# Kernel optimization log

Hardware: AMD Instinct MI355X
Metric: run time of the kernel (lower is better)

Reference implementation:

```python
import jax, jax.numpy as jnp
import numpy as np

N_NODES = 20000
N_EDGES = 640000
N_GRAPHS = 64
HID = 256
NF = 128
NG = 100   # edge_channels / num_gaussians
NBLK = 6
CUTOFF = 10.0
LOG2 = float(np.log(2.0))


def setup_inputs() -> dict:
    key = jax.random.key(0)
    ks = jax.random.split(key, 24)
    inp = {}
    inp['atom_types'] = jax.random.randint(ks[0], (N_NODES,), 0, 100)
    inp['edge_index'] = jax.random.randint(ks[1], (2, N_EDGES), 0, N_NODES)
    inp['edge_length'] = jax.random.uniform(ks[2], (N_EDGES, 1), jnp.float32) * CUTOFF
    inp['batch_seg'] = jnp.sort(jax.random.randint(ks[3], (N_NODES,), 0, N_GRAPHS))
    s = 0.05
    # embedding table (Embedding(100, hidden); init small so max_norm=10 renorm is inactive)
    inp['atom_emb'] = jax.random.normal(ks[4], (100, HID), jnp.float32) * 0.5
    # per-interaction-block params, stacked on a leading block axis; weights stored [in, out]
    inp['W1s'] = jax.random.normal(ks[5], (NBLK, NG, NF), jnp.float32) * s      # filter MLP lin1
    inp['b1s'] = jnp.zeros((NBLK, NF), jnp.float32)
    inp['W2s'] = jax.random.normal(ks[6], (NBLK, NF, NF), jnp.float32) * s      # filter MLP lin2
    inp['b2s'] = jnp.zeros((NBLK, NF), jnp.float32)
    inp['lin1Ws'] = jax.random.normal(ks[7], (NBLK, HID, NF), jnp.float32) * s  # CFConv.lin1 (no bias)
    inp['lin2Ws'] = jax.random.normal(ks[8], (NBLK, NF, HID), jnp.float32) * s  # CFConv.lin2
    inp['lin2bs'] = jnp.zeros((NBLK, HID), jnp.float32)
    inp['linWs'] = jax.random.normal(ks[9], (NBLK, HID, HID), jnp.float32) * s  # InteractionBlock.lin
    inp['linbs'] = jnp.zeros((NBLK, HID), jnp.float32)
    # final MLP: Linear(256,256) -> act -> Linear(256,256)
    inp['fW1'] = jax.random.normal(ks[10], (HID, HID), jnp.float32) * s
    inp['fb1'] = jnp.zeros((HID,), jnp.float32)
    inp['fW2'] = jax.random.normal(ks[11], (HID, HID), jnp.float32) * s
    inp['fb2'] = jnp.zeros((HID,), jnp.float32)
    return inp


def _ssp(x):
    # ShiftedSoftplus: softplus(x) - log(2)
    return jax.nn.softplus(x) - LOG2


def reference(atom_emb, W1s, b1s, W2s, b2s, lin1Ws, lin2Ws, lin2bs, linWs, linbs,
              fW1, fb1, fW2, fb2, edge_length, atom_types, edge_index, batch_seg):
    n = atom_types.shape[0]
    h = atom_emb[atom_types]                                     # [N, H]
    # Gaussian smearing edge encoder: exp(-0.5/dg^2 * (d - mu_k)^2)
    offsets = jnp.linspace(0.0, CUTOFF, NG)
    coeff = -0.5 / (offsets[1] - offsets[0]) ** 2
    edge_attr = jnp.exp(coeff * (edge_length - offsets[None, :]) ** 2)  # [E, NG]
    # smooth=False cutoff gate
    C = (edge_length <= CUTOFF).astype(h.dtype)                  # [E, 1]
    src, dst = edge_index[0], edge_index[1]
    for i in range(NBLK):
        W = _ssp(edge_attr @ W1s[i] + b1s[i]) @ W2s[i] + b2s[i]  # [E, F]
        W = W * C
        xf = h @ lin1Ws[i]                                       # [N, F]
        msg = xf[src] * W                                        # gather + filter: [E, F]
        agg = jax.ops.segment_sum(msg, dst, num_segments=n)      # scatter-add: [N, F]
        hc = _ssp(agg @ lin2Ws[i] + lin2bs[i])
        hc = hc @ linWs[i] + linbs[i]
        h = h + hc                                               # residual
    pooled = jax.ops.segment_max(h, batch_seg, num_segments=N_GRAPHS)  # global_max_pool
    out = jax.nn.relu(pooled @ fW1 + fb1) @ fW2 + fb2
    return out
```

## Files before the change

kernel.cpp:

```cpp
#include <hip/hip_runtime.h>
#include <math.h>

#define HID 256
#define NF 128
#define NGAUSS 100
#define NBLK 6
#define NGRAPH 64
#define CUTOFF_F 10.0f
#define T_TAB 2048

typedef __attribute__((ext_vector_type(8))) short bf16x8;
typedef __attribute__((ext_vector_type(4))) float f32x4;

__device__ __forceinline__ float ssp(float x) {
    return fmaxf(x, 0.0f) + log1pf(expf(-fabsf(x))) - 0.69314718056f;
}
__device__ __forceinline__ short f2bf(float f) {
    unsigned u = __float_as_uint(f);
    u = u + 0x7fffu + ((u >> 16) & 1u);
    return (short)(u >> 16);
}
__device__ __forceinline__ float bf2f(unsigned s) {
    return __uint_as_float(s << 16);
}
__device__ __forceinline__ unsigned enc_f(float f) {
    unsigned b = __float_as_uint(f);
    return (b & 0x80000000u) ? ~b : (b | 0x80000000u);
}
__device__ __forceinline__ float dec_f(unsigned u) {
    unsigned b = (u & 0x80000000u) ? (u & 0x7FFFFFFFu) : ~u;
    return __uint_as_float(b);
}

__global__ __launch_bounds__(256) void transpose_bf(
        const float* __restrict__ in, short* __restrict__ out,
        int K_src, int K_pad, int C)
{
    int i = blockIdx.y;
    int idx = blockIdx.x * 256 + threadIdx.x;
    if (idx >= K_pad * C) return;
    int k = idx / C, c = idx % C;
    out[((size_t)i * C + c) * K_pad + k] =
        (k < K_src) ? f2bf(in[((size_t)i * K_src + k) * C + c]) : (short)0;
}

__global__ __launch_bounds__(256) void build_table_mfma(
        const short* __restrict__ W1T, const float* __restrict__ b1s,
        const short* __restrict__ W2T, const float* __restrict__ b2s,
        short* __restrict__ Wtab)
{
    __shared__ short Gs[32 * NF];
    __shared__ short Hs[32 * NF];
    char* gb = (char*)Gs;
    char* hb = (char*)Hs;
    const int i = blockIdx.y;
    const int r0 = blockIdx.x * 32;
    const int wv = threadIdx.x >> 6, lane = threadIdx.x & 63;
    const int lrow = lane & 15, lgrp = lane >> 4;

    const float delta = CUTOFF_F / 99.0f;
    const float coeff = -0.5f / (delta * delta);
    for (int idx = threadIdx.x; idx < 32 * NF; idx += 256) {
        int row = idx >> 7, k = idx & 127;
        float d = (float)(r0 + row) * (CUTOFF_F / (float)(T_TAB - 1));
        float x = d - (float)k * delta;
        float v = (k < NGAUSS) ? expf(coeff * x * x) : 0.0f;
        int byte = idx * 2;
        byte ^= (row & 7) << 4;
        *(short*)(gb + byte) = f2bf(v);
    }
    __syncthreads();

    f32x4 zero = {0.0f, 0.0f, 0.0f, 0.0f};
    f32x4 c1[2][2] = {{zero, zero}, {zero, zero}};
    for (int s = 0; s < 4; ++s) {
        bf16x8 a[2], b[2];
        #pragma unroll
        for (int m = 0; m < 2; ++m) {
            int row = m * 16 + lrow;
            int byte = (row * NF + s * 32 + lgrp * 8) * 2;
            byte ^= (row & 7) << 4;
            a[m] = *(const bf16x8*)(gb + byte);
        }
        #pragma unroll
        for (int n = 0; n < 2; ++n) {
            int col = wv * 32 + n * 16 + lrow;
            b[n] = *(const bf16x8*)(W1T + ((size_t)i * NF + col) * NF + s * 32 + lgrp * 8);
        }
        #pragma unroll
        for (int m = 0; m < 2; ++m)
            #pragma unroll
            for (int n = 0; n < 2; ++n)
                c1[m][n] = __builtin_amdgcn_mfma_f32_16x16x32_bf16(a[m], b[n], c1[m][n], 0, 0, 0);
    }
    #pragma unroll
    for (int m = 0; m < 2; ++m)
        #pragma unroll
        for (int n = 0; n < 2; ++n) {
            int col = wv * 32 + n * 16 + lrow;
            float bb = b1s[i * NF + col];
            #pragma unroll
            for (int j = 0; j < 4; ++j) {
                int row = m * 16 + lgrp * 4 + j;
                int byte = (row * NF + col) * 2;
                byte ^= (row & 7) << 4;
                *(short*)(hb + byte) = f2bf(ssp(c1[m][n][j] + bb));
            }
        }
    __syncthreads();

    f32x4 c2[2][2] = {{zero, zero}, {zero, zero}};
    for (int s = 0; s < 4; ++s) {
        bf16x8 a[2], b[2];
        #pragma unroll
        for (int m = 0; m < 2; ++m) {
            int row = m * 16 + lrow;
            int byte = (row * NF + s * 32 + lgrp * 8) * 2;
            byte ^= (row & 7) << 4;
            a[m] = *(const bf16x8*)(hb + byte);
        }
        #pragma unroll
        for (int n = 0; n < 2; ++n) {
            int col = wv * 32 + n * 16 + lrow;
            b[n] = *(const bf16x8*)(W2T + ((size_t)i * NF + col) * NF + s * 32 + lgrp * 8);
        }
        #pragma unroll
        for (int m = 0; m < 2; ++m)
            #pragma unroll
            for (int n = 0; n < 2; ++n)
                c2[m][n] = __builtin_amdgcn_mfma_f32_16x16x32_bf16(a[m], b[n], c2[m][n], 0, 0, 0);
    }
    #pragma unroll
    for (int m = 0; m < 2; ++m)
        #pragma unroll
        for (int n = 0; n < 2; ++n) {
            int col = wv * 32 + n * 16 + lrow;
            float bb = b2s[i * NF + col];
            #pragma unroll
            for (int j = 0; j < 4; ++j) {
                int t = r0 + m * 16 + lgrp * 4 + j;
                Wtab[((size_t)i * T_TAB + t) * NF + col] = f2bf(c2[m][n][j] + bb);
            }
        }
}

__global__ __launch_bounds__(256) void pack_wtab(
        const short* __restrict__ Wtab, uint2* __restrict__ WtabP)
{
    size_t idx = (size_t)blockIdx.x * 256 + threadIdx.x;
    if (idx >= (size_t)NBLK * (T_TAB + 1) * 64) return;
    int l = (int)(idx & 63);
    int t = (int)((idx >> 6) % (T_TAB + 1));
    int i = (int)(idx / ((size_t)64 * (T_TAB + 1)));
    if (t == T_TAB) { WtabP[idx] = make_uint2(0u, 0u); return; }
    int t1 = (t + 1 < T_TAB) ? t + 1 : t;
    unsigned a = *((const unsigned*)(Wtab + ((size_t)i * T_TAB + t)  * NF) + l);
    unsigned b = *((const unsigned*)(Wtab + ((size_t)i * T_TAB + t1) * NF) + l);
    WtabP[idx] = make_uint2(a, b);
}

__global__ __launch_bounds__(256) void embed_k(
        const float* __restrict__ emb, const int* __restrict__ types,
        float* __restrict__ h, int N)
{
    int gid = blockIdx.x * 256 + threadIdx.x;
    if (gid >= N * HID) return;
    int n = gid >> 8, c = gid & (HID - 1);
    h[gid] = emb[(size_t)types[n] * HID + c];
}

__global__ __launch_bounds__(256) void hist_k(
        const int* __restrict__ dst, int* __restrict__ hist, int E)
{
    int e = blockIdx.x * 256 + threadIdx.x;
    if (e < E) atomicAdd(&hist[dst[e]], 1);
}

__global__ __launch_bounds__(1024) void scan_k(
        const int* __restrict__ in, int* __restrict__ out, int n)
{
    __shared__ int wsum[16];
    __shared__ int carry_s;
    const int tid = threadIdx.x, lane = tid & 63, w = tid >> 6;
    if (tid == 0) carry_s = 0;
    __syncthreads();
    for (int base = 0; base < n; base += 1024) {
        int i = base + tid;
        int v = (i < n) ? in[i] : 0;
        int s = v;
        #pragma unroll
        for (int d = 1; d < 64; d <<= 1) {
            int t = __shfl_up(s, d);
            if (lane >= d) s += t;
        }
        if (lane == 63) wsum[w] = s;
        __syncthreads();
        if (w == 0 && lane < 16) {
            int ws = wsum[lane];
            #pragma unroll
            for (int d = 1; d < 16; d <<= 1) {
                int t = __shfl_up(ws, d);
                if (lane >= d) ws += t;
            }
            wsum[lane] = ws;
        }
        __syncthreads();
        int carry = carry_s;
        if (i < n) out[i] = carry + (w ? wsum[w - 1] : 0) + s - v;
        __syncthreads();
        if (tid == 1023) carry_s = carry + wsum[15];
        __syncthreads();
    }
    if (threadIdx.x == 0) out[n] = carry_s;
}

__global__ __launch_bounds__(256) void scatter_k(
        const int* __restrict__ src, const int* __restrict__ dst,
        const float* __restrict__ elen, const int* __restrict__ off,
        int* __restrict__ cursor, unsigned long long* __restrict__ csr_pk, int E)
{
    int e = blockIdx.x * 256 + threadIdx.x;
    if (e >= E) return;
    int t = dst[e];
    int pos = off[t] + atomicAdd(&cursor[t], 1);
    float d = elen[e];
    float u = d * ((float)(T_TAB - 1) / CUTOFF_F);
    u = fminf(fmaxf(u, 0.0f), (float)(T_TAB - 1) - 1e-3f);
    u = (d <= CUTOFF_F) ? u : (float)T_TAB;
    csr_pk[pos] = ((unsigned long long)__float_as_uint(u) << 32) | (unsigned)src[e];
}

__global__ __launch_bounds__(256) void sort_k(
        const int* __restrict__ off, unsigned long long* __restrict__ csr_pk, int N)
{
    const int node = (blockIdx.x * 256 + threadIdx.x) >> 6;
    const int lane = threadIdx.x & 63;
    if (node >= N) return;
    const int beg = off[node], end = off[node + 1];
    const int deg = end - beg;
    if (deg <= 1) return;
    if (deg <= 128) {
        const unsigned long long PAD = ~0ull;
        unsigned long long v0 = (lane < deg) ? csr_pk[beg + lane] : PAD;
        unsigned long long v1 = (64 + lane < deg) ? csr_pk[beg + 64 + lane] : PAD;
        if (deg > 64) {
            for (int size = 2; size <= 128; size <<= 1)
                for (int stride = size >> 1; stride > 0; stride >>= 1) {
                    if (stride == 64) {
                        unsigned long long lo = v0 < v1 ? v0 : v1;
                        unsigned long long hi = v0 < v1 ? v1 : v0;
                        v0 = lo; v1 = hi;
                    } else {
                        unsigned long long p0 = __shfl_xor(v0, stride);
                        unsigned long long p1 = __shfl_xor(v1, stride);
                        bool up = (lane & stride) != 0;
                        bool d0 = ((lane & size) == 0);
                        bool d1 = (((lane + 64) & size) == 0);
                        v0 = (up ^ d0) ? (v0 < p0 ? v0 : p0) : (v0 > p0 ? v0 : p0);
                        v1 = (up ^ d1) ? (v1 < p1 ? v1 : p1) : (v1 > p1 ? v1 : p1);
                    }
                }
            if (lane < deg) csr_pk[beg + lane] = v0;
            if (64 + lane < deg) csr_pk[beg + 64 + lane] = v1;
        } else {
            for (int size = 2; size <= 64; size <<= 1)
                for (int stride = size >> 1; stride > 0; stride >>= 1) {
                    unsigned long long p0 = __shfl_xor(v0, stride);
                    bool up = (lane & stride) != 0;
                    bool d0 = ((lane & size) == 0);
                    v0 = (up ^ d0) ? (v0 < p0 ? v0 : p0) : (v0 > p0 ? v0 : p0);
                }
            if (lane < deg) csr_pk[beg + lane] = v0;
        }
    } else if (lane == 0) {
        for (int a = beg + 1; a < end; ++a) {
            unsigned long long key = csr_pk[a];
            int b = a - 1;
            while (b >= beg && csr_pk[b] > key) { csr_pk[b + 1] = csr_pk[b]; --b; }
            csr_pk[b + 1] = key;
        }
    }
}


__global__ __launch_bounds__(256) void lin1_k(
        const float* __restrict__ h, const short* __restrict__ lin1T,
        short* __restrict__ xf, int N)
{
    const int wv = threadIdx.x >> 6, lane = threadIdx.x & 63;
    const int lrow = lane & 15, lgrp = lane >> 4;
    const int wrow = wv >> 1, wcol = wv & 1;
    const int r0 = blockIdx.x * 64 + wrow * 32;

    f32x4 zero = {0.0f, 0.0f, 0.0f, 0.0f};
    f32x4 c[2][4] = {{zero, zero, zero, zero}, {zero, zero, zero, zero}};

    for (int s = 0; s < 8; ++s) {
        bf16x8 a[2], b[4];
        #pragma unroll
        for (int m = 0; m < 2; ++m) {
            int row = r0 + m * 16 + lrow;
            if (row >= N) row = N - 1;
            const float* hp = h + (size_t)row * HID + s * 32 + lgrp * 8;
            float4 p0 = *(const float4*)hp;
            float4 p1 = *(const float4*)(hp + 4);
            bf16x8 t;
            t[0] = f2bf(p0.x); t[1] = f2bf(p0.y); t[2] = f2bf(p0.z); t[3] = f2bf(p0.w);
            t[4] = f2bf(p1.x); t[5] = f2bf(p1.y); t[6] = f2bf(p1.z); t[7] = f2bf(p1.w);
            a[m] = t;
        }
        #pragma unroll
        for (int n = 0; n < 4; ++n) {
            int col = wcol * 64 + n * 16 + lrow;
            b[n] = *(const bf16x8*)(lin1T + (size_t)col * HID + s * 32 + lgrp * 8);
        }
        #pragma unroll
        for (int m = 0; m < 2; ++m)
            #pragma unroll
            for (int n = 0; n < 4; ++n)
                c[m][n] = __builtin_amdgcn_mfma_f32_16x16x32_bf16(a[m], b[n], c[m][n], 0, 0, 0);
    }
    #pragma unroll
    for (int m = 0; m < 2; ++m)
        #pragma unroll
        for (int n = 0; n < 4; ++n) {
            int col = wcol * 64 + n * 16 + lrow;
            #pragma unroll
            for (int j = 0; j < 4; ++j) {
                int row = r0 + m * 16 + lgrp * 4 + j;
                if (row < N) xf[(size_t)row * NF + col] = f2bf(c[m][n][j]);
            }
        }
}

__global__ __launch_bounds__(256) void agg_k(
        const short* __restrict__ xf, const uint2* __restrict__ wt,
        const int* __restrict__ off, const unsigned long long* __restrict__ csr_pk,
        short* __restrict__ agg, int N)
{
    const int node = (blockIdx.x * 256 + threadIdx.x) >> 6;
    const int lane = threadIdx.x & 63;
    if (node >= N) return;
    const int beg = __builtin_amdgcn_readfirstlane(off[node]);
    const int end = __builtin_amdgcn_readfirstlane(off[node + 1]);
    float a0 = 0.0f, a1 = 0.0f;

    int k = beg;
    for (; k + 8 <= end; k += 8) {
        unsigned long long pk[8];
        #pragma unroll
        for (int q = 0; q < 8; ++q) pk[q] = csr_pk[k + q];
        uint2 wp[8];
        unsigned xv[8];
        float fr[8];
        #pragma unroll
        for (int q = 0; q < 8; ++q) {
            int s = (int)(unsigned)pk[q];
            float uf = __uint_as_float((unsigned)(pk[q] >> 32));
            int i0 = (int)uf;
            fr[q] = uf - (float)i0;
            wp[q] = wt[(size_t)i0 * 64 + lane];
            xv[q] = *(const unsigned*)(xf + (size_t)s * NF + 2 * lane);
        }
        #pragma unroll
        for (int q = 0; q < 8; ++q) {
            float w0a = bf2f(wp[q].x & 0xffffu), w0b = bf2f(wp[q].x >> 16);
            float w1a = bf2f(wp[q].y & 0xffffu), w1b = bf2f(wp[q].y >> 16);
            float xa  = bf2f(xv[q] & 0xffffu), xb  = bf2f(xv[q] >> 16);
            a0 = fmaf(xa, fmaf(fr[q], w1a - w0a, w0a), a0);
            a1 = fmaf(xb, fmaf(fr[q], w1b - w0b, w0b), a1);
        }
    }
    if (k < end) {
        const int rem = end - k;
        unsigned long long pk[8];
        #pragma unroll
        for (int q = 0; q < 8; ++q) {
            int kk = k + q < end ? k + q : end - 1;
            pk[q] = csr_pk[kk];
        }
        uint2 wp[8];
        unsigned xv[8];
        float fr[8];
        #pragma unroll
        for (int q = 0; q < 8; ++q) {
            int s = (int)(unsigned)pk[q];
            float uf = __uint_as_float((unsigned)(pk[q] >> 32));
            int i0 = (int)uf;
            fr[q] = uf - (float)i0;
            wp[q] = wt[(size_t)i0 * 64 + lane];
            xv[q] = *(const unsigned*)(xf + (size_t)s * NF + 2 * lane);
        }
        #pragma unroll
        for (int q = 0; q < 8; ++q) {
            float g = (q < rem) ? 1.0f : 0.0f;
            float w0a = bf2f(wp[q].x & 0xffffu), w0b = bf2f(wp[q].x >> 16);
            float w1a = bf2f(wp[q].y & 0xffffu), w1b = bf2f(wp[q].y >> 16);
            float xa  = bf2f(xv[q] & 0xffffu), xb  = bf2f(xv[q] >> 16);
            a0 = fmaf(xa * g, fmaf(fr[q], w1a - w0a, w0a), a0);
            a1 = fmaf(xb * g, fmaf(fr[q], w1b - w0b, w0b), a1);
        }
    }
    unsigned pack = (unsigned)(unsigned short)f2bf(a0)
                  | ((unsigned)(unsigned short)f2bf(a1) << 16);
    *(unsigned*)(agg + (size_t)node * NF + 2 * lane) = pack;
}

__global__ __launch_bounds__(512) void update_k(
        const short* __restrict__ aggb, const short* __restrict__ W2T,
        const float* __restrict__ b2, const short* __restrict__ W3T,
        const float* __restrict__ b3, float* __restrict__ h,
        const short* __restrict__ lin1Tn, short* __restrict__ xf_out, int N)
{
    __shared__ short tmp[32 * HID];
    __shared__ float ftmp[32][HID + 4];
    char* tb = (char*)tmp;
    const int wv = threadIdx.x >> 6, lane = threadIdx.x & 63;
    const int lrow = lane & 15, lgrp = lane >> 4;
    const int r0 = blockIdx.x * 32;

    f32x4 zero = {0.0f, 0.0f, 0.0f, 0.0f};
    f32x4 c1[2][2] = {{zero, zero}, {zero, zero}};

    for (int s = 0; s < 4; ++s) {
        bf16x8 a[2], b[2];
        #pragma unroll
        for (int m = 0; m < 2; ++m) {
            int row = r0 + m * 16 + lrow;
            if (row >= N) row = N - 1;
            a[m] = *(const bf16x8*)(aggb + (size_t)row * NF + s * 32 + lgrp * 8);
        }
        #pragma unroll
        for (int n = 0; n < 2; ++n) {
            int col = wv * 32 + n * 16 + lrow;
            b[n] = *(const bf16x8*)(W2T + (size_t)col * NF + s * 32 + lgrp * 8);
        }
        #pragma unroll
        for (int m = 0; m < 2; ++m)
            #pragma unroll
            for (int n = 0; n < 2; ++n)
                c1[m][n] = __builtin_amdgcn_mfma_f32_16x16x32_bf16(a[m], b[n], c1[m][n], 0, 0, 0);
    }
    #pragma unroll
    for (int m = 0; m < 2; ++m)
        #pragma unroll
        for (int n = 0; n < 2; ++n) {
            int col = wv * 32 + n * 16 + lrow;
            float bb = b2[col];
            #pragma unroll
            for (int j = 0; j < 4; ++j) {
                int row = m * 16 + lgrp * 4 + j;
                int byte = (row * HID + col) * 2;
                byte ^= (row & 7) << 4;
                *(short*)(tb + byte) = f2bf(ssp(c1[m][n][j] + bb));
            }
        }
    __syncthreads();

    f32x4 c2[2][2] = {{zero, zero}, {zero, zero}};
    for (int s = 0; s < 8; ++s) {
        bf16x8 a[2], b[2];
        #pragma unroll
        for (int m = 0; m < 2; ++m) {
            int row = m * 16 + lrow;
            int byte = (row * HID + s * 32 + lgrp * 8) * 2;
            byte ^= (row & 7) << 4;
            a[m] = *(const bf16x8*)(tb + byte);
        }
        #pragma unroll
        for (int n = 0; n < 2; ++n) {
            int col = wv * 32 + n * 16 + lrow;
            b[n] = *(const bf16x8*)(W3T + (size_t)col * HID + s * 32 + lgrp * 8);
        }
        #pragma unroll
        for (int m = 0; m < 2; ++m)
            #pragma unroll
            for (int n = 0; n < 2; ++n)
                c2[m][n] = __builtin_amdgcn_mfma_f32_16x16x32_bf16(a[m], b[n], c2[m][n], 0, 0, 0);
    }

    #pragma unroll
    for (int m = 0; m < 2; ++m)
        #pragma unroll
        for (int n = 0; n < 2; ++n) {
            int col = wv * 32 + n * 16 + lrow;
            float bb = b3[col];
            #pragma unroll
            for (int j = 0; j < 4; ++j)
                ftmp[m * 16 + lgrp * 4 + j][col] = c2[m][n][j] + bb;
        }
    __syncthreads();

    {
        const int r  = threadIdx.x >> 4;
        const int c0 = (threadIdx.x & 15) * 4;
        const int row = r0 + r;
        const bool valid = row < N;
        float* hp = h + (size_t)row * HID;
        #pragma unroll
        for (int k = 0; k < 4; ++k) {
            int col = c0 + k * 64;
            float4 hv = valid ? *(const float4*)(hp + col)
                              : make_float4(0.f, 0.f, 0.f, 0.f);
            float4 f = *(const float4*)&ftmp[r][col];
            hv.x += f.x; hv.y += f.y; hv.z += f.z; hv.w += f.w;
            if (valid) *(float4*)(hp + col) = hv;
            short4 s4;
            s4.x = f2bf(hv.x); s4.y = f2bf(hv.y); s4.z = f2bf(hv.z); s4.w = f2bf(hv.w);
            int byte = (r * HID + col) * 2;
            byte ^= (r & 7) << 4;
            *(short4*)(tb + byte) = s4;
        }
    }
    if (xf_out == nullptr) return;
    __syncthreads();

    f32x4 c3[2] = {zero, zero};
    for (int s = 0; s < 8; ++s) {
        bf16x8 a[2], b;
        #pragma unroll
        for (int m = 0; m < 2; ++m) {
            int row = m * 16 + lrow;
            int byte = (row * HID + s * 32 + lgrp * 8) * 2;
            byte ^= (row & 7) << 4;
            a[m] = *(const bf16x8*)(tb + byte);
        }
        {
            int col = wv * 16 + lrow;
            b = *(const bf16x8*)(lin1Tn + (size_t)col * HID + s * 32 + lgrp * 8);
        }
        #pragma unroll
        for (int m = 0; m < 2; ++m)
            c3[m] = __builtin_amdgcn_mfma_f32_16x16x32_bf16(a[m], b, c3[m], 0, 0, 0);
    }
    #pragma unroll
    for (int m = 0; m < 2; ++m) {
        int col = wv * 16 + lrow;
        #pragma unroll
        for (int j = 0; j < 4; ++j) {
            int row = r0 + m * 16 + lgrp * 4 + j;
            if (row < N) xf_out[(size_t)row * NF + col] = f2bf(c3[m][j]);
        }
    }
}

__global__ __launch_bounds__(256) void pool_init(unsigned* __restrict__ pe)
{
    int i = blockIdx.x * 256 + threadIdx.x;
    if (i < NGRAPH * HID) pe[i] = enc_f(-INFINITY);
}

__global__ __launch_bounds__(256) void pool_max2(
        const float* __restrict__ h, const int* __restrict__ seg,
        unsigned* __restrict__ pe, int N)
{
    const int c = threadIdx.x;
    const int base = blockIdx.x * 64;
    if (base >= N) return;
    int cur = seg[base];
    float m = -INFINITY;
    for (int r = 0; r < 64; ++r) {
        int row = base + r;
        if (row >= N) break;
        int s = seg[row];
        if (s != cur) {
            atomicMax(&pe[(size_t)cur * HID + c], enc_f(m));
            m = -INFINITY;
            cur = s;
        }
        m = fmaxf(m, h[(size_t)row * HID + c]);
    }
    atomicMax(&pe[(size_t)cur * HID + c], enc_f(m));
}

__global__ __launch_bounds__(1024) void final_mlp(
        const unsigned* __restrict__ pe,
        const float* __restrict__ fW1, const float* __restrict__ fb1,
        const float* __restrict__ fW2, const float* __restrict__ fb2,
        float* __restrict__ out)
{
    __shared__ float p[HID];
    __shared__ float part[4][HID];
    __shared__ float p2[HID];
    const int g = blockIdx.x;
    const int c = threadIdx.x & 255;
    const int kq = threadIdx.x >> 8;
    if (threadIdx.x < HID) p[threadIdx.x] = dec_f(pe[(size_t)g * HID + threadIdx.x]);
    __syncthreads();
    float a = 0.0f;
    #pragma unroll 8
    for (int k = kq * 64; k < kq * 64 + 64; ++k)
        a = fmaf(p[k], fW1[(size_t)k * HID + c], a);
    part[kq][c] = a;
    __syncthreads();
    if (kq == 0) {
        float s = part[0][c] + part[1][c] + part[2][c] + part[3][c] + fb1[c];
        p2[c] = fmaxf(s, 0.0f);
    }
    __syncthreads();
    float o = 0.0f;
    #pragma unroll 8
    for (int k = kq * 64; k < kq * 64 + 64; ++k)
        o = fmaf(p2[k], fW2[(size_t)k * HID + c], o);
    part[kq][c] = o;
    __syncthreads();
    if (kq == 0)
        out[(size_t)g * HID + c] = part[0][c] + part[1][c] + part[2][c] + part[3][c] + fb2[c];
}

extern "C" void kernel_launch(void* const* d_in, const int* in_sizes, int n_in,
                              void* d_out, int out_size, void* d_ws, size_t ws_size,
                              hipStream_t stream)
{
    const int*   atom_types = (const int*)  d_in[0];
    const int*   edge_index = (const int*)  d_in[1];
    const float* edge_len   = (const float*)d_in[2];
    const int*   batch_seg  = (const int*)  d_in[3];
    const float* atom_emb   = (const float*)d_in[4];
    const float* W1s    = (const float*)d_in[5];
    const float* b1s    = (const float*)d_in[6];
    const float* W2s    = (const float*)d_in[7];
    const float* b2s    = (const float*)d_in[8];
    const float* lin1Ws = (const float*)d_in[9];
    const float* lin2Ws = (const float*)d_in[10];
    const float* lin2bs = (const float*)d_in[11];
    const float* linWs  = (const float*)d_in[12];
    const float* linbs  = (const float*)d_in[13];
    const float* fW1    = (const float*)d_in[14];
    const float* fb1    = (const float*)d_in[15];
    const float* fW2    = (const float*)d_in[16];
    const float* fb2    = (const float*)d_in[17];

    const int N = in_sizes[0];
    const int E = in_sizes[1] / 2;
    const int* src = edge_index;
    const int* dst = edge_index + E;

    char* ws = (char*)d_ws;
    float* h     = (float*)ws;  ws += (size_t)N * HID * sizeof(float);
    short* xf    = (short*)ws;  ws += (size_t)N * NF * sizeof(short);
    short* aggb  = (short*)ws;  ws += (size_t)N * NF * sizeof(short);
    short* Wtab  = (short*)ws;  ws += (size_t)NBLK * T_TAB * NF * sizeof(short);
    uint2* WtabP = (uint2*)ws;  ws += (size_t)NBLK * (T_TAB + 1) * 64 * sizeof(uint2);
    short* lin1T = (short*)ws;  ws += (size_t)NBLK * NF * HID * sizeof(short);
    short* W2T   = (short*)ws;  ws += (size_t)NBLK * HID * NF * sizeof(short);
    short* W3T   = (short*)ws;  ws += (size_t)NBLK * HID * HID * sizeof(short);
    short* W1Tb  = (short*)ws;  ws += (size_t)NBLK * NF * NF * sizeof(short);
    short* W2Tb  = (short*)ws;  ws += (size_t)NBLK * NF * NF * sizeof(short);
    unsigned* pooled = (unsigned*)ws;   ws += (size_t)NGRAPH * HID * sizeof(unsigned);
    unsigned long long* csr_pk = (unsigned long long*)ws; ws += (size_t)E * sizeof(unsigned long long);
    int* hist    = (int*)ws;  ws += (size_t)N * sizeof(int);
    int* off     = (int*)ws;  ws += (size_t)(N + 1) * sizeof(int);
    int* cursor  = (int*)ws;

    hipMemsetAsync(hist, 0, (size_t)N * sizeof(int), stream);
    hipMemsetAsync(cursor, 0, (size_t)N * sizeof(int), stream);
    hist_k<<<(E + 255) / 256, 256, 0, stream>>>(dst, hist, E);
    scan_k<<<1, 1024, 0, stream>>>(hist, off, N);
    scatter_k<<<(E + 255) / 256, 256, 0, stream>>>(src, dst, edge_len, off,
                                                   cursor, csr_pk, E);
    sort_k<<<(N * 64 + 255) / 256, 256, 0, stream>>>(off, csr_pk, N);

    transpose_bf<<<dim3((NF * NF + 255) / 256, NBLK), 256, 0, stream>>>(W1s, W1Tb, NGAUSS, NF, NF);
    transpose_bf<<<dim3((NF * NF + 255) / 256, NBLK), 256, 0, stream>>>(W2s, W2Tb, NF, NF, NF);
    transpose_bf<<<dim3((HID * NF + 255) / 256, NBLK), 256, 0, stream>>>(lin1Ws, lin1T, HID, HID, NF);
    transpose_bf<<<dim3((NF * HID + 255) / 256, NBLK), 256, 0, stream>>>(lin2Ws, W2T, NF, NF, HID);
    transpose_bf<<<dim3((HID * HID + 255) / 256, NBLK), 256, 0, stream>>>(linWs, W3T, HID, HID, HID);

    build_table_mfma<<<dim3(T_TAB / 32, NBLK), 256, 0, stream>>>(W1Tb, b1s, W2Tb, b2s, Wtab);
    pack_wtab<<<(int)(((size_t)NBLK * (T_TAB + 1) * 64 + 255) / 256), 256, 0, stream>>>(Wtab, WtabP);
    embed_k<<<(N * HID + 255) / 256, 256, 0, stream>>>(atom_emb, atom_types, h, N);
    lin1_k<<<(N + 63) / 64, 256, 0, stream>>>(h, lin1T, xf, N);

    for (int i = 0; i < NBLK; ++i) {
        agg_k<<<(N * 64 + 255) / 256, 256, 0, stream>>>(
            xf, WtabP + (size_t)i * (T_TAB + 1) * 64, off, csr_pk, aggb, N);
        update_k<<<(N + 31) / 32, 512, 0, stream>>>(
            aggb, W2T + (size_t)i * HID * NF, lin2bs + (size_t)i * HID,
            W3T + (size_t)i * HID * HID, linbs + (size_t)i * HID, h,
            lin1T + (size_t)(i + 1) * NF * HID,
            (i < NBLK - 1) ? xf : nullptr, N);
    }

    pool_init<<<(NGRAPH * HID + 255) / 256, 256, 0, stream>>>(pooled);
    pool_max2<<<(N + 63) / 64, 256, 0, stream>>>(h, batch_seg, pooled, N);
    final_mlp<<<NGRAPH, 1024, 0, stream>>>(pooled, fW1, fb1, fW2, fb2, (float*)d_out);
}
```

Baseline: 603.2 us.

## Fuse edge aggregation into per-block update kernel via swizzled LDS staging

Merges the gather/aggregate kernel into the node update kernel: each 512-thread block first aggregates its 32 nodes (4 per wave) into an XOR-swizzled shared-memory tile, then runs the MFMA update directly from LDS. This removes the global round trip of the bf16 aggregate buffer and one kernel launch per interaction block. xf is now double-buffered, because blocks read neighbours' xf while others write the next one. The cost is lower parallelism for the latency-bound gather: fewer waves per node set and more LDS and registers per block, which may reduce occupancy.

Result: slower. 723.4 us (+19.9%).

```diff
diff --git a/kernel.cpp b/kernel.cpp
--- a/kernel.cpp
+++ b/kernel.cpp
@@ -333,92 +333,94 @@
         }
 }
 
-__global__ __launch_bounds__(256) void agg_k(
-        const short* __restrict__ xf, const uint2* __restrict__ wt,
+__global__ __launch_bounds__(512) void block_k(
+        const short* __restrict__ xf_in, const uint2* __restrict__ wt,
         const int* __restrict__ off, const unsigned long long* __restrict__ csr_pk,
-        short* __restrict__ agg, int N)
-{
-    const int node = (blockIdx.x * 256 + threadIdx.x) >> 6;
-    const int lane = threadIdx.x & 63;
-    if (node >= N) return;
-    const int beg = __builtin_amdgcn_readfirstlane(off[node]);
-    const int end = __builtin_amdgcn_readfirstlane(off[node + 1]);
-    float a0 = 0.0f, a1 = 0.0f;
-
-    int k = beg;
-    for (; k + 8 <= end; k += 8) {
-        unsigned long long pk[8];
-        #pragma unroll
-        for (int q = 0; q < 8; ++q) pk[q] = csr_pk[k + q];
-        uint2 wp[8];
-        unsigned xv[8];
-        float fr[8];
-        #pragma unroll
-        for (int q = 0; q < 8; ++q) {
-            int s = (int)(unsigned)pk[q];
-            float uf = __uint_as_float((unsigned)(pk[q] >> 32));
-            int i0 = (int)uf;
-            fr[q] = uf - (float)i0;
-            wp[q] = wt[(size_t)i0 * 64 + lane];
-            xv[q] = *(const unsigned*)(xf + (size_t)s * NF + 2 * lane);
-        }
-        #pragma unroll
-        for (int q = 0; q < 8; ++q) {
-            float w0a = bf2f(wp[q].x & 0xffffu), w0b = bf2f(wp[q].x >> 16);
-            float w1a = bf2f(wp[q].y & 0xffffu), w1b = bf2f(wp[q].y >> 16);
-            float xa  = bf2f(xv[q] & 0xffffu), xb  = bf2f(xv[q] >> 16);
-            a0 = fmaf(xa, fmaf(fr[q], w1a - w0a, w0a), a0);
-            a1 = fmaf(xb, fmaf(fr[q], w1b - w0b, w0b), a1);
-        }
-    }
-    if (k < end) {
-        const int rem = end - k;
-        unsigned long long pk[8];
-        #pragma unroll
-        for (int q = 0; q < 8; ++q) {
-            int kk = k + q < end ? k + q : end - 1;
-            pk[q] = csr_pk[kk];
-        }
-        uint2 wp[8];
-        unsigned xv[8];
-        float fr[8];
-        #pragma unroll
-        for (int q = 0; q < 8; ++q) {
-            int s = (int)(unsigned)pk[q];
-            float uf = __uint_as_float((unsigned)(pk[q] >> 32));
-            int i0 = (int)uf;
-            fr[q] = uf - (float)i0;
-            wp[q] = wt[(size_t)i0 * 64 + lane];
-            xv[q] = *(const unsigned*)(xf + (size_t)s * NF + 2 * lane);
-        }
-        #pragma unroll
-        for (int q = 0; q < 8; ++q) {
-            float g = (q < rem) ? 1.0f : 0.0f;
-            float w0a = bf2f(wp[q].x & 0xffffu), w0b = bf2f(wp[q].x >> 16);
-            float w1a = bf2f(wp[q].y & 0xffffu), w1b = bf2f(wp[q].y >> 16);
-            float xa  = bf2f(xv[q] & 0xffffu), xb  = bf2f(xv[q] >> 16);
-            a0 = fmaf(xa * g, fmaf(fr[q], w1a - w0a, w0a), a0);
-            a1 = fmaf(xb * g, fmaf(fr[q], w1b - w0b, w0b), a1);
-        }
-    }
-    unsigned pack = (unsigned)(unsigned short)f2bf(a0)
-                  | ((unsigned)(unsigned short)f2bf(a1) << 16);
-    *(unsigned*)(agg + (size_t)node * NF + 2 * lane) = pack;
-}
-
-__global__ __launch_bounds__(512) void update_k(
-        const short* __restrict__ aggb, const short* __restrict__ W2T,
-        const float* __restrict__ b2, const short* __restrict__ W3T,
-        const float* __restrict__ b3, float* __restrict__ h,
-        const short* __restrict__ lin1Tn, short* __restrict__ xf_out, int N)
+        const short* __restrict__ W2T, const float* __restrict__ b2,
+        const short* __restrict__ W3T, const float* __restrict__ b3,
+        float* __restrict__ h, const short* __restrict__ lin1Tn,
+        short* __restrict__ xf_out, int N)
 {
     __shared__ short tmp[32 * HID];
     __shared__ float ftmp[32][HID + 4];
     char* tb = (char*)tmp;
+    char* ab = (char*)ftmp;
     const int wv = threadIdx.x >> 6, lane = threadIdx.x & 63;
     const int lrow = lane & 15, lgrp = lane >> 4;
     const int r0 = blockIdx.x * 32;
 
+    for (int t = 0; t < 4; ++t) {
+        const int node = r0 + wv * 4 + t;
+        float a0 = 0.0f, a1 = 0.0f;
+        if (node < N) {
+            const int beg = __builtin_amdgcn_readfirstlane(off[node]);
+            const int end = __builtin_amdgcn_readfirstlane(off[node + 1]);
+            int k = beg;
+            for (; k + 8 <= end; k += 8) {
+                unsigned long long pk[8];
+                #pragma unroll
+                for (int q = 0; q < 8; ++q) pk[q] = csr_pk[k + q];
+                uint2 wp[8];
+                unsigned xv[8];
+                float fr[8];
+                #pragma unroll
+                for (int q = 0; q < 8; ++q) {
+                    int s = (int)(unsigned)pk[q];
+                    float uf = __uint_as_float((unsigned)(pk[q] >> 32));
+                    int i0 = (int)uf;
+                    fr[q] = uf - (float)i0;
+                    wp[q] = wt[(size_t)i0 * 64 + lane];
+                    xv[q] = *(const unsigned*)(xf_in + (size_t)s * NF + 2 * lane);
+                }
+                #pragma unroll
+                for (int q = 0; q < 8; ++q) {
+                    float w0a = bf2f(wp[q].x & 0xffffu), w0b = bf2f(wp[q].x >> 16);
+                    float w1a = bf2f(wp[q].y & 0xffffu), w1b = bf2f(wp[q].y >> 16);
+                    float xa  = bf2f(xv[q] & 0xffffu), xb  = bf2f(xv[q] >> 16);
+                    a0 = fmaf(xa, fmaf(fr[q], w1a - w0a, w0a), a0);
+                    a1 = fmaf(xb, fmaf(fr[q], w1b - w0b, w0b), a1);
+                }
+            }
+            if (k < end) {
+                const int rem = end - k;
+                unsigned long long pk[8];
+                #pragma unroll
+                for (int q = 0; q < 8; ++q) {
+                    int kk = k + q < end ? k + q : end - 1;
+                    pk[q] = csr_pk[kk];
+                }
+                uint2 wp[8];
+                unsigned xv[8];
+                float fr[8];
+                #pragma unroll
+                for (int q = 0; q < 8; ++q) {
+                    int s = (int)(unsigned)pk[q];
+                    float uf = __uint_as_float((unsigned)(pk[q] >> 32));
+                    int i0 = (int)uf;
+                    fr[q] = uf - (float)i0;
+                    wp[q] = wt[(size_t)i0 * 64 + lane];
+                    xv[q] = *(const unsigned*)(xf_in + (size_t)s * NF + 2 * lane);
+                }
+                #pragma unroll
+                for (int q = 0; q < 8; ++q) {
+                    float g = (q < rem) ? 1.0f : 0.0f;
+                    float w0a = bf2f(wp[q].x & 0xffffu), w0b = bf2f(wp[q].x >> 16);
+                    float w1a = bf2f(wp[q].y & 0xffffu), w1b = bf2f(wp[q].y >> 16);
+                    float xa  = bf2f(xv[q] & 0xffffu), xb  = bf2f(xv[q] >> 16);
+                    a0 = fmaf(xa * g, fmaf(fr[q], w1a - w0a, w0a), a0);
+                    a1 = fmaf(xb * g, fmaf(fr[q], w1b - w0b, w0b), a1);
+                }
+            }
+        }
+        unsigned pack = (unsigned)(unsigned short)f2bf(a0)
+                      | ((unsigned)(unsigned short)f2bf(a1) << 16);
+        const int row = wv * 4 + t;
+        int byte = (row * NF + 2 * lane) * 2;
+        byte ^= (row & 7) << 4;
+        *(unsigned*)(ab + byte) = pack;
+    }
+    __syncthreads();
+
     f32x4 zero = {0.0f, 0.0f, 0.0f, 0.0f};
     f32x4 c1[2][2] = {{zero, zero}, {zero, zero}};
 
@@ -426,9 +428,10 @@
         bf16x8 a[2], b[2];
         #pragma unroll
         for (int m = 0; m < 2; ++m) {
-            int row = r0 + m * 16 + lrow;
-            if (row >= N) row = N - 1;
-            a[m] = *(const bf16x8*)(aggb + (size_t)row * NF + s * 32 + lgrp * 8);
+            int row = m * 16 + lrow;
+            int byte = (row * NF + s * 32 + lgrp * 8) * 2;
+            byte ^= (row & 7) << 4;
+            a[m] = *(const bf16x8*)(ab + byte);
         }
         #pragma unroll
         for (int n = 0; n < 2; ++n) {
@@ -638,8 +641,8 @@
 
     char* ws = (char*)d_ws;
     float* h     = (float*)ws;  ws += (size_t)N * HID * sizeof(float);
-    short* xf    = (short*)ws;  ws += (size_t)N * NF * sizeof(short);
-    short* aggb  = (short*)ws;  ws += (size_t)N * NF * sizeof(short);
+    short* xf0   = (short*)ws;  ws += (size_t)N * NF * sizeof(short);
+    short* xf1   = (short*)ws;  ws += (size_t)N * NF * sizeof(short);
     short* Wtab  = (short*)ws;  ws += (size_t)NBLK * T_TAB * NF * sizeof(short);
     uint2* WtabP = (uint2*)ws;  ws += (size_t)NBLK * (T_TAB + 1) * 64 * sizeof(uint2);
     short* lin1T = (short*)ws;  ws += (size_t)NBLK * NF * HID * sizeof(short);
@@ -670,16 +673,17 @@
     build_table_mfma<<<dim3(T_TAB / 32, NBLK), 256, 0, stream>>>(W1Tb, b1s, W2Tb, b2s, Wtab);
     pack_wtab<<<(int)(((size_t)NBLK * (T_TAB + 1) * 64 + 255) / 256), 256, 0, stream>>>(Wtab, WtabP);
     embed_k<<<(N * HID + 255) / 256, 256, 0, stream>>>(atom_emb, atom_types, h, N);
-    lin1_k<<<(N + 63) / 64, 256, 0, stream>>>(h, lin1T, xf, N);
+    lin1_k<<<(N + 63) / 64, 256, 0, stream>>>(h, lin1T, xf0, N);
 
     for (int i = 0; i < NBLK; ++i) {
-        agg_k<<<(N * 64 + 255) / 256, 256, 0, stream>>>(
-            xf, WtabP + (size_t)i * (T_TAB + 1) * 64, off, csr_pk, aggb, N);
-        update_k<<<(N + 31) / 32, 512, 0, stream>>>(
-            aggb, W2T + (size_t)i * HID * NF, lin2bs + (size_t)i * HID,
+        short* xin  = (i & 1) ? xf1 : xf0;
+        short* xout = (i & 1) ? xf0 : xf1;
+        block_k<<<(N + 31) / 32, 512, 0, stream>>>(
+            xin, WtabP + (size_t)i * (T_TAB + 1) * 64, off, csr_pk,
+            W2T + (size_t)i * HID * NF, lin2bs + (size_t)i * HID,
             W3T + (size_t)i * HID * HID, linbs + (size_t)i * HID, h,
             lin1T + (size_t)(i + 1) * NF * HID,
-            (i < NBLK - 1) ? xf : nullptr, N);
+            (i < NBLK - 1) ? xout : nullptr, N);
     }
 
     pool_init<<<(NGRAPH * HID + 255) / 256, 256, 0, stream>>>(pooled);
```
